# Kernel optimization log

Hardware: AMD Instinct MI355X
Metric: run time of the kernel (lower is better)

The kernel has to match this reference:

```python
import jax, jax.numpy as jnp
import numpy as np

LN_EPS = 1e-12


def setup_inputs() -> dict:
    key = jax.random.key(0)
    ks = jax.random.split(key, 10)
    B, S, W, D, H = 16, 512, 5, 200, 768
    std = 0.02
    return {
        "layer_output": jax.random.normal(ks[0], (B, S, H), dtype=jnp.float32),
        "word_embeddings": jax.random.normal(ks[1], (B, S, W, D), dtype=jnp.float32),
        "word_mask": jax.random.randint(ks[2], (B, S, W), 0, 2, dtype=jnp.int64),
        "W1": jax.random.normal(ks[3], (D, H), dtype=jnp.float32) * std,
        "b1": jnp.zeros((H,), dtype=jnp.float32),
        "W2": jax.random.normal(ks[4], (H, H), dtype=jnp.float32) * std,
        "b2": jnp.zeros((H,), dtype=jnp.float32),
        "attn_W": jax.random.normal(ks[5], (H, H), dtype=jnp.float32) * std,
        "ln_gamma": jnp.ones((H,), dtype=jnp.float32),
        "ln_beta": jnp.zeros((H,), dtype=jnp.float32),
    }


def reference(layer_output, word_embeddings, word_mask, W1, b1, W2, b2, attn_W, ln_gamma, ln_beta):
    # word_transform: Linear -> Tanh -> Linear (dropout = identity in eval)
    we = jnp.tanh(jnp.einsum("bswd,dh->bswh", word_embeddings, W1) + b1)
    we = jnp.einsum("bswh,hk->bswk", we, W2) + b2  # [B,S,W,H]

    # bilinear word attention: (x @ attn_W) . word_outputs -> score over W
    q = jnp.einsum("bsh,hk->bsk", layer_output, attn_W)  # [B,S,H]
    alpha = jnp.einsum("bsk,bswk->bsw", q, we)            # [B,S,W]
    alpha = alpha + (1.0 - word_mask.astype(alpha.dtype)) * -10000.0
    alpha = jax.nn.softmax(alpha, axis=-1)

    # weighted sum over words + residual
    agg = jnp.einsum("bsw,bswh->bsh", alpha, we)
    h = layer_output + agg

    # LayerNorm (fuse_layer; dropout = identity in eval)
    mu = jnp.mean(h, axis=-1, keepdims=True)
    var = jnp.mean(jnp.square(h - mu), axis=-1, keepdims=True)
    return (h - mu) * jax.lax.rsqrt(var + LN_EPS) * ln_gamma + ln_beta
```

## Files before the change

### kernel.cpp

```cpp
#include <hip/hip_runtime.h>
#include <hip/hip_bf16.h>
#include <math.h>


typedef __attribute__((ext_vector_type(8))) short bf16x8;
typedef __attribute__((ext_vector_type(4))) float f32x4;

__device__ __forceinline__ unsigned short f2bf_bits(float f) {
    __hip_bfloat16 h = __float2bfloat16(f);
    return *reinterpret_cast<unsigned short*>(&h);
}
__device__ __forceinline__ float bf_bits2f(unsigned short u) {
    union { unsigned int i; float f; } v; v.i = ((unsigned int)u) << 16; return v.f;
}
__device__ __forceinline__ float tanh_fast(float x) {
    float xc = fminf(fmaxf(x, -9.f), 9.f);
    float t  = __expf(2.f * xc);
    return (t - 1.f) * __builtin_amdgcn_rcpf(t + 1.f);
}

__device__ __forceinline__ void async_cp16(const void* g, void* lds) {
#if __has_builtin(__builtin_amdgcn_global_load_lds)
    auto gp = (const __attribute__((address_space(1))) unsigned int*)g;
    auto lp = (__attribute__((address_space(3))) unsigned int*)lds;
    __builtin_amdgcn_global_load_lds(gp, lp, 16, 0, 0);
#else
    *(uint4*)lds = *(const uint4*)g;
#endif
}

template<bool HAS_BIAS, bool TANH_ACT, bool RESID, bool OUT_BF16, int N, int K, int GX>
__global__ __launch_bounds__(256) void mfma_gemm(
    const __hip_bfloat16* __restrict__ A,
    const __hip_bfloat16* __restrict__ Bt,
    const float* __restrict__ bias,
    const float* __restrict__ resid,
    void* __restrict__ outp)
{
    __shared__ __align__(16) unsigned char smem[32768];
    unsigned short* As = (unsigned short*)smem;
    unsigned short* Bs = (unsigned short*)(smem + 8192);

    int bx, by;
    {
        const int total = gridDim.x;
        const int per_xcd = total >> 3;
        if ((total & 7) == 0 && (per_xcd % GX) == 0) {
            int xcd = blockIdx.x & 7, idx = blockIdx.x >> 3;
            int lin = xcd * per_xcd + idx;
            by = lin / GX; bx = lin % GX;
        } else { by = blockIdx.x / GX; bx = blockIdx.x % GX; }
    }
    const int m0 = by * 128;
    const int n0 = bx * 128;

    const int tid  = threadIdx.x;
    const int lane = tid & 63;
    const int wave = tid >> 6;
    const int wm   = wave & 1;
    const int wn   = wave >> 1;

    const int srow  = lane >> 2;
    const int skoff = (lane & 3) * 8;
    const __hip_bfloat16* gA = A  + (size_t)(m0 + wave * 32 + srow) * K + skoff;
    const __hip_bfloat16* gB = Bt + (size_t)(n0 + wave * 32 + srow) * K + skoff;
    unsigned short* lA = As + wave * 1024 + lane * 8;
    unsigned short* lB = Bs + wave * 1024 + lane * 8;

    const int row16 = lane & 15;
    const int kq    = lane >> 4;

    f32x4 acc[4][4];
#pragma unroll
    for (int i = 0; i < 4; i++)
#pragma unroll
        for (int j = 0; j < 4; j++) acc[i][j] = (f32x4){0.f, 0.f, 0.f, 0.f};

    for (int k0 = 0; k0 < K; k0 += 32) {
        async_cp16(gA,          lA);
        async_cp16(gA + 16 * K, lA + 512);
        async_cp16(gB,          lB);
        async_cp16(gB + 16 * K, lB + 512);
        gA += 32; gB += 32;
        __syncthreads();

        bf16x8 af[4], bg[4];
#pragma unroll
        for (int mi = 0; mi < 4; mi++)
            af[mi] = *(const bf16x8*)&As[(wm * 64 + mi * 16 + row16) * 32 + kq * 8];
#pragma unroll
        for (int ni = 0; ni < 4; ni++)
            bg[ni] = *(const bf16x8*)&Bs[(wn * 64 + ni * 16 + row16) * 32 + kq * 8];
#pragma unroll
        for (int mi = 0; mi < 4; mi++)
#pragma unroll
            for (int ni = 0; ni < 4; ni++)
                acc[mi][ni] = __builtin_amdgcn_mfma_f32_16x16x32_bf16(
                    af[mi], bg[ni], acc[mi][ni], 0, 0, 0);
        __syncthreads();
    }

    if (OUT_BF16) {
        unsigned short* rep = (unsigned short*)smem;
#pragma unroll
        for (int ni = 0; ni < 4; ni++) {
            const int c = wn * 64 + ni * 16 + row16;
            float bcol = HAS_BIAS ? bias[n0 + c] : 0.f;
#pragma unroll
            for (int mi = 0; mi < 4; mi++)
#pragma unroll
                for (int r = 0; r < 4; r++) {
                    const int rr = wm * 64 + mi * 16 + kq * 4 + r;
                    float v = acc[mi][ni][r];
                    if (HAS_BIAS) v += bcol;
                    if (TANH_ACT) v = tanh_fast(v);
                    rep[rr * 128 + c] = f2bf_bits(v);
                }
        }
        __syncthreads();
#pragma unroll
        for (int p = 0; p < 8; p++) {
            const int lin = p * 256 + tid;
            const int row = lin >> 4;
            const int c8  = lin & 15;
            uint4 d = *(const uint4*)&rep[row * 128 + c8 * 8];
            *(uint4*)((__hip_bfloat16*)outp + (size_t)(m0 + row) * N + n0 + c8 * 8) = d;
        }
    } else {
        float* rep = (float*)smem;
#pragma unroll
        for (int h = 0; h < 2; h++) {
            if (wm == h) {
#pragma unroll
                for (int ni = 0; ni < 4; ni++) {
                    const int c = wn * 64 + ni * 16 + row16;
                    float bcol = HAS_BIAS ? bias[n0 + c] : 0.f;
#pragma unroll
                    for (int mi = 0; mi < 4; mi++)
#pragma unroll
                        for (int r = 0; r < 4; r++) {
                            const int rr = mi * 16 + kq * 4 + r;
                            float v = acc[mi][ni][r];
                            if (HAS_BIAS) v += bcol;
                            if (TANH_ACT) v = tanh_fast(v);
                            rep[rr * 128 + c] = v;
                        }
                }
            }
            __syncthreads();
#pragma unroll
            for (int p = 0; p < 8; p++) {
                const int lin = p * 256 + tid;
                const int row = lin >> 5;
                const int c4  = lin & 31;
                float4 v = *(const float4*)&rep[row * 128 + c4 * 4];
                const int grow = m0 + h * 64 + row;
                if (RESID) {
                    float4 rv = *(const float4*)&resid[(size_t)grow * N + n0 + c4 * 4];
                    v.x += rv.x; v.y += rv.y; v.z += rv.z; v.w += rv.w;
                }
                *(float4*)((float*)outp + (size_t)grow * N + n0 + c4 * 4) = v;
            }
            __syncthreads();
        }
    }
}

__global__ __launch_bounds__(256) void cvt_all(
    const float* __restrict__ x,  __hip_bfloat16* __restrict__ xb,
    const float* __restrict__ w2, __hip_bfloat16* __restrict__ w2b,
    const float* __restrict__ aw, __hip_bfloat16* __restrict__ awb)
{
    const int NX = 8192 * 768 / 4;
    const int NW = 768 * 768 / 4;
    long long i = (long long)blockIdx.x * 256 + threadIdx.x;
    const float* src; __hip_bfloat16* dst;
    if (i < NX)           { src = x;  dst = xb;  }
    else if (i < NX + NW) { src = w2; dst = w2b; i -= NX; }
    else                  { src = aw; dst = awb; i -= NX + NW; if (i >= NW) return; }
    float4 v = ((const float4*)src)[i];
    ((ushort4*)dst)[i] = make_ushort4(f2bf_bits(v.x), f2bf_bits(v.y), f2bf_bits(v.z), f2bf_bits(v.w));
}

__global__ __launch_bounds__(256) void cvt_padE(const float* __restrict__ E,
                                                __hip_bfloat16* __restrict__ Eb)
{
    const int lane = threadIdx.x & 63;
    const int wave = threadIdx.x >> 6;
    const long long row = (long long)blockIdx.x * 4 + wave;
    const int k = lane * 4;
    if (k < 224) {
        float4 v = make_float4(0.f, 0.f, 0.f, 0.f);
        if (k < 200) v = *(const float4*)&E[row * 200 + k];
        *(ushort4*)&Eb[row * 224 + k] =
            make_ushort4(f2bf_bits(v.x), f2bf_bits(v.y), f2bf_bits(v.z), f2bf_bits(v.w));
    }
}

__global__ __launch_bounds__(256) void transpose_cvt(const float* __restrict__ in,
                                                     __hip_bfloat16* __restrict__ out,
                                                     int R, int C, int Rpad)
{
    __shared__ float tile[32][33];
    const int c0 = blockIdx.x * 32, r0 = blockIdx.y * 32;
    const int x = threadIdx.x, y = threadIdx.y;
#pragma unroll
    for (int i = 0; i < 32; i += 8) {
        int r = r0 + y + i;
        tile[y + i][x] = (r < R) ? in[(size_t)r * C + c0 + x] : 0.f;
    }
    __syncthreads();
#pragma unroll
    for (int i = 0; i < 32; i += 8)
        out[(size_t)(c0 + y + i) * Rpad + r0 + x] = __float2bfloat16(tile[x][y + i]);
}

__global__ __launch_bounds__(256) void attn_kernel(
    const __hip_bfloat16* __restrict__ T,
    const __hip_bfloat16* P,
    const int* __restrict__ mask,
    __hip_bfloat16* S)
{
    const int lane = threadIdx.x & 63;
    const int wave = threadIdx.x >> 6;
    const int r    = blockIdx.x * 4 + wave;
    const int base = lane * 12;

    float pv[12];
    {
        const ushort4* pp = (const ushort4*)((const unsigned short*)P + (size_t)r * 768 + base);
        ushort4 u0 = pp[0], u1 = pp[1], u2 = pp[2];
        unsigned short us[12] = {u0.x,u0.y,u0.z,u0.w, u1.x,u1.y,u1.z,u1.w, u2.x,u2.y,u2.z,u2.w};
#pragma unroll
        for (int j = 0; j < 12; j++) pv[j] = bf_bits2f(us[j]);
    }
    float tv[5][12], part[5];
#pragma unroll
    for (int w = 0; w < 5; w++) {
        const ushort4* tp = (const ushort4*)((const unsigned short*)T + ((size_t)r * 5 + w) * 768 + base);
        ushort4 u0 = tp[0], u1 = tp[1], u2 = tp[2];
        unsigned short us[12] = {u0.x,u0.y,u0.z,u0.w, u1.x,u1.y,u1.z,u1.w, u2.x,u2.y,u2.z,u2.w};
        float s = 0.f;
#pragma unroll
        for (int j = 0; j < 12; j++) { tv[w][j] = bf_bits2f(us[j]); s += tv[w][j] * pv[j]; }
        part[w] = s;
    }
#pragma unroll
    for (int off = 32; off > 0; off >>= 1)
#pragma unroll
        for (int w = 0; w < 5; w++)
            part[w] += __shfl_xor(part[w], off, 64);

    float logit[5], mx = -1e30f;
#pragma unroll
    for (int w = 0; w < 5; w++) {
        float m = (float)mask[(size_t)r * 5 + w];
        logit[w] = part[w] - 10000.0f * (1.0f - m);
        mx = fmaxf(mx, logit[w]);
    }
    float se = 0.f;
#pragma unroll
    for (int w = 0; w < 5; w++) { logit[w] = expf(logit[w] - mx); se += logit[w]; }
    const float inv = 1.0f / se;

    unsigned short os[12];
#pragma unroll
    for (int j = 0; j < 12; j++) {
        float s = 0.f;
#pragma unroll
        for (int w = 0; w < 5; w++) s += logit[w] * tv[w][j];
        os[j] = f2bf_bits(s * inv);
    }
    ushort4* sp = (ushort4*)((unsigned short*)S + (size_t)r * 768 + base);
    sp[0] = make_ushort4(os[0], os[1], os[2],  os[3]);
    sp[1] = make_ushort4(os[4], os[5], os[6],  os[7]);
    sp[2] = make_ushort4(os[8], os[9], os[10], os[11]);
}

__global__ __launch_bounds__(256) void ln_kernel(
    const float* __restrict__ Hbuf, const float* __restrict__ gamma,
    const float* __restrict__ beta, float* __restrict__ out)
{
    const int lane = threadIdx.x & 63;
    const int wave = threadIdx.x >> 6;
    const int r    = blockIdx.x * 4 + wave;
    const float* hr = Hbuf + (size_t)r * 768 + lane * 12;

    float v[12];
    {
        float4 a = *(const float4*)(hr);
        float4 b = *(const float4*)(hr + 4);
        float4 c = *(const float4*)(hr + 8);
        v[0]=a.x; v[1]=a.y; v[2]=a.z; v[3]=a.w;
        v[4]=b.x; v[5]=b.y; v[6]=b.z; v[7]=b.w;
        v[8]=c.x; v[9]=c.y; v[10]=c.z; v[11]=c.w;
    }
    float s = 0.f;
#pragma unroll
    for (int j = 0; j < 12; j++) s += v[j];
#pragma unroll
    for (int off = 32; off > 0; off >>= 1) s += __shfl_xor(s, off, 64);
    const float mu = s * (1.f / 768.f);
    float vs = 0.f;
#pragma unroll
    for (int j = 0; j < 12; j++) { float d = v[j] - mu; vs += d * d; }
#pragma unroll
    for (int off = 32; off > 0; off >>= 1) vs += __shfl_xor(vs, off, 64);
    const float rs = rsqrtf(vs * (1.f / 768.f) + 1e-12f);

    float o[12];
#pragma unroll
    for (int j = 0; j < 12; j++) {
        int h = lane * 12 + j;
        o[j] = (v[j] - mu) * rs * gamma[h] + beta[h];
    }
    float* orow = out + (size_t)r * 768 + lane * 12;
    *(float4*)(orow)     = make_float4(o[0], o[1], o[2],  o[3]);
    *(float4*)(orow + 4) = make_float4(o[4], o[5], o[6],  o[7]);
    *(float4*)(orow + 8) = make_float4(o[8], o[9], o[10], o[11]);
}

extern "C" void kernel_launch(void* const* d_in, const int* in_sizes, int n_in,
                              void* d_out, int out_size, void* d_ws, size_t ws_size,
                              hipStream_t stream)
{
    const float* x      = (const float*)d_in[0];
    const float* E      = (const float*)d_in[1];
    const int*   mask   = (const int*)d_in[2];
    const float* W1     = (const float*)d_in[3];
    const float* b1     = (const float*)d_in[4];
    const float* W2     = (const float*)d_in[5];
    const float* b2     = (const float*)d_in[6];
    const float* attn_W = (const float*)d_in[7];
    const float* gamma  = (const float*)d_in[8];
    const float* beta   = (const float*)d_in[9];
    float* out = (float*)d_out;

    const int BS = 8192, H = 768, M1 = 40960, KP = 224;

    char* p = (char*)d_ws;
    auto alloc = [&](size_t bytes) { char* q = p; p += (bytes + 255) & ~(size_t)255; return q; };
    __hip_bfloat16* xb    = (__hip_bfloat16*)alloc((size_t)BS * H * 2);
    __hip_bfloat16* W2b   = (__hip_bfloat16*)alloc((size_t)H * H * 2);
    __hip_bfloat16* W2Tb  = (__hip_bfloat16*)alloc((size_t)H * H * 2);
    __hip_bfloat16* attnb = (__hip_bfloat16*)alloc((size_t)H * H * 2);
    __hip_bfloat16* Ctb   = (__hip_bfloat16*)alloc((size_t)H * H * 2);
    __hip_bfloat16* W1Tb  = (__hip_bfloat16*)alloc((size_t)H * KP * 2);
    __hip_bfloat16* Tb    = (__hip_bfloat16*)alloc((size_t)M1 * H * 2);
    __hip_bfloat16* Eb    = (__hip_bfloat16*)alloc((size_t)M1 * KP * 2);
    float* Hb = (float*)Tb;
    __hip_bfloat16* Pb = Eb;
    __hip_bfloat16* Sb = Pb;

    cvt_all<<<6144 + 576 + 576, 256, 0, stream>>>(x, xb, W2, W2b, attn_W, attnb);
    cvt_padE<<<M1 / 4, 256, 0, stream>>>(E, Eb);
    transpose_cvt<<<dim3(24, 7),  dim3(32, 8), 0, stream>>>(W1, W1Tb, 200, H, KP);
    transpose_cvt<<<dim3(24, 24), dim3(32, 8), 0, stream>>>(W2, W2Tb, H, H, H);

    mfma_gemm<false, false, false, true, 768, 768, 6><<<36, 256, 0, stream>>>(
        W2b, attnb, nullptr, nullptr, Ctb);
    mfma_gemm<true, true, false, true, 768, 224, 6><<<1920, 256, 0, stream>>>(
        Eb, W1Tb, b1, nullptr, Tb);
    mfma_gemm<false, false, false, true, 768, 768, 6><<<384, 256, 0, stream>>>(
        xb, Ctb, nullptr, nullptr, Pb);
    attn_kernel<<<BS / 4, 256, 0, stream>>>(Tb, Pb, mask, Sb);
    mfma_gemm<true, false, true, false, 768, 768, 6><<<384, 256, 0, stream>>>(
        Sb, W2Tb, b2, x, Hb);
    ln_kernel<<<BS / 4, 256, 0, stream>>>(Hb, gamma, beta, out);
}
```

Measured before the change: 242.1 us.

## Deepen GEMM K-tile to 64 with XOR-swizzled LDS and fuse prep kernels

```diff
diff --git a/kernel.cpp b/kernel.cpp
--- a/kernel.cpp
+++ b/kernel.cpp
@@ -39,7 +39,7 @@
 {
     __shared__ __align__(16) unsigned char smem[32768];
     unsigned short* As = (unsigned short*)smem;
-    unsigned short* Bs = (unsigned short*)(smem + 8192);
+    unsigned short* Bs = (unsigned short*)(smem + 16384);
 
     int bx, by;
     {
@@ -60,12 +60,13 @@
     const int wm   = wave & 1;
     const int wn   = wave >> 1;
 
-    const int srow  = lane >> 2;
-    const int skoff = (lane & 3) * 8;
-    const __hip_bfloat16* gA = A  + (size_t)(m0 + wave * 32 + srow) * K + skoff;
-    const __hip_bfloat16* gB = Bt + (size_t)(n0 + wave * 32 + srow) * K + skoff;
-    unsigned short* lA = As + wave * 1024 + lane * 8;
-    unsigned short* lB = Bs + wave * 1024 + lane * 8;
+    const int rsub = lane >> 3;
+    const int slot = lane & 7;
+    const int kc   = slot ^ rsub;
+    const __hip_bfloat16* gA = A  + (size_t)(m0 + wave * 32 + rsub) * K + kc * 8;
+    const __hip_bfloat16* gB = Bt + (size_t)(n0 + wave * 32 + rsub) * K + kc * 8;
+    unsigned short* lA = As + wave * 2048 + lane * 8;
+    unsigned short* lB = Bs + wave * 2048 + lane * 8;
 
     const int row16 = lane & 15;
     const int kq    = lane >> 4;
@@ -76,27 +77,39 @@
 #pragma unroll
         for (int j = 0; j < 4; j++) acc[i][j] = (f32x4){0.f, 0.f, 0.f, 0.f};
 
-    for (int k0 = 0; k0 < K; k0 += 32) {
-        async_cp16(gA,          lA);
-        async_cp16(gA + 16 * K, lA + 512);
-        async_cp16(gB,          lB);
-        async_cp16(gB + 16 * K, lB + 512);
-        gA += 32; gB += 32;
+    for (int k0 = 0; k0 < K; k0 += 64) {
+#pragma unroll
+        for (int i = 0; i < 4; i++) {
+            async_cp16(gA + i * 8 * K, lA + i * 512);
+            async_cp16(gB + i * 8 * K, lB + i * 512);
+        }
+        gA += 64; gB += 64;
         __syncthreads();
 
-        bf16x8 af[4], bg[4];
-#pragma unroll
-        for (int mi = 0; mi < 4; mi++)
-            af[mi] = *(const bf16x8*)&As[(wm * 64 + mi * 16 + row16) * 32 + kq * 8];
-#pragma unroll
-        for (int ni = 0; ni < 4; ni++)
-            bg[ni] = *(const bf16x8*)&Bs[(wn * 64 + ni * 16 + row16) * 32 + kq * 8];
-#pragma unroll
-        for (int mi = 0; mi < 4; mi++)
-#pragma unroll
-            for (int ni = 0; ni < 4; ni++)
-                acc[mi][ni] = __builtin_amdgcn_mfma_f32_16x16x32_bf16(
-                    af[mi], bg[ni], acc[mi][ni], 0, 0, 0);
+        bf16x8 af[2][4], bg[2][4];
+#pragma unroll
+        for (int kh = 0; kh < 2; kh++) {
+#pragma unroll
+            for (int mi = 0; mi < 4; mi++) {
+                const int r = wm * 64 + mi * 16 + row16;
+                const int s = (kh * 4 + kq) ^ (r & 7);
+                af[kh][mi] = *(const bf16x8*)&As[r * 64 + s * 8];
+            }
+#pragma unroll
+            for (int ni = 0; ni < 4; ni++) {
+                const int r = wn * 64 + ni * 16 + row16;
+                const int s = (kh * 4 + kq) ^ (r & 7);
+                bg[kh][ni] = *(const bf16x8*)&Bs[r * 64 + s * 8];
+            }
+        }
+#pragma unroll
+        for (int kh = 0; kh < 2; kh++)
+#pragma unroll
+            for (int mi = 0; mi < 4; mi++)
+#pragma unroll
+                for (int ni = 0; ni < 4; ni++)
+                    acc[mi][ni] = __builtin_amdgcn_mfma_f32_16x16x32_bf16(
+                        af[kh][mi], bg[kh][ni], acc[mi][ni], 0, 0, 0);
         __syncthreads();
     }
 
@@ -166,53 +179,47 @@
     }
 }
 
-__global__ __launch_bounds__(256) void cvt_all(
+__global__ __launch_bounds__(256) void prep_kernel(
     const float* __restrict__ x,  __hip_bfloat16* __restrict__ xb,
     const float* __restrict__ w2, __hip_bfloat16* __restrict__ w2b,
-    const float* __restrict__ aw, __hip_bfloat16* __restrict__ awb)
-{
-    const int NX = 8192 * 768 / 4;
-    const int NW = 768 * 768 / 4;
-    long long i = (long long)blockIdx.x * 256 + threadIdx.x;
-    const float* src; __hip_bfloat16* dst;
-    if (i < NX)           { src = x;  dst = xb;  }
-    else if (i < NX + NW) { src = w2; dst = w2b; i -= NX; }
-    else                  { src = aw; dst = awb; i -= NX + NW; if (i >= NW) return; }
-    float4 v = ((const float4*)src)[i];
-    ((ushort4*)dst)[i] = make_ushort4(f2bf_bits(v.x), f2bf_bits(v.y), f2bf_bits(v.z), f2bf_bits(v.w));
-}
-
-__global__ __launch_bounds__(256) void cvt_padE(const float* __restrict__ E,
-                                                __hip_bfloat16* __restrict__ Eb)
-{
-    const int lane = threadIdx.x & 63;
-    const int wave = threadIdx.x >> 6;
-    const long long row = (long long)blockIdx.x * 4 + wave;
-    const int k = lane * 4;
-    if (k < 224) {
+    const float* __restrict__ aw, __hip_bfloat16* __restrict__ awb,
+    const float* __restrict__ E,  __hip_bfloat16* __restrict__ Eb,
+    const float* __restrict__ W1, __hip_bfloat16* __restrict__ W1Tb,
+    __hip_bfloat16* __restrict__ W2Tb)
+{
+    __shared__ float tile[32][33];
+    const int b = blockIdx.x, tid = threadIdx.x;
+    if (b < 6144 + 576 + 576) {
+        const float* src; __hip_bfloat16* dst; long long i;
+        if (b < 6144)      { src = x;  dst = xb;  i = (long long)b * 256 + tid; }
+        else if (b < 6720) { src = w2; dst = w2b; i = (long long)(b - 6144) * 256 + tid; }
+        else               { src = aw; dst = awb; i = (long long)(b - 6720) * 256 + tid; }
+        float4 v = ((const float4*)src)[i];
+        ((ushort4*)dst)[i] = make_ushort4(f2bf_bits(v.x), f2bf_bits(v.y), f2bf_bits(v.z), f2bf_bits(v.w));
+    } else if (b < 7296 + 10240) {
+        const int lane = tid & 63, wave = tid >> 6;
+        const long long row = (long long)(b - 7296) * 4 + wave;
+        const int k = lane * 4;
         float4 v = make_float4(0.f, 0.f, 0.f, 0.f);
         if (k < 200) v = *(const float4*)&E[row * 200 + k];
-        *(ushort4*)&Eb[row * 224 + k] =
+        *(ushort4*)&Eb[row * 256 + k] =
             make_ushort4(f2bf_bits(v.x), f2bf_bits(v.y), f2bf_bits(v.z), f2bf_bits(v.w));
-    }
-}
-
-__global__ __launch_bounds__(256) void transpose_cvt(const float* __restrict__ in,
-                                                     __hip_bfloat16* __restrict__ out,
-                                                     int R, int C, int Rpad)
-{
-    __shared__ float tile[32][33];
-    const int c0 = blockIdx.x * 32, r0 = blockIdx.y * 32;
-    const int x = threadIdx.x, y = threadIdx.y;
-#pragma unroll
-    for (int i = 0; i < 32; i += 8) {
-        int r = r0 + y + i;
-        tile[y + i][x] = (r < R) ? in[(size_t)r * C + c0 + x] : 0.f;
-    }
-    __syncthreads();
-#pragma unroll
-    for (int i = 0; i < 32; i += 8)
-        out[(size_t)(c0 + y + i) * Rpad + r0 + x] = __float2bfloat16(tile[x][y + i]);
+    } else {
+        const float* in; __hip_bfloat16* outb; int R, C, Rpad, t;
+        if (b < 17536 + 192) { t = b - 17536; in = W1; outb = W1Tb; R = 200; C = 768; Rpad = 256; }
+        else                 { t = b - 17728; in = w2; outb = W2Tb; R = 768; C = 768; Rpad = 768; }
+        const int c0 = (t % 24) * 32, r0 = (t / 24) * 32;
+        const int xx = tid & 31, yy = tid >> 5;
+#pragma unroll
+        for (int i = 0; i < 32; i += 8) {
+            int r = r0 + yy + i;
+            tile[yy + i][xx] = (r < R) ? in[(size_t)r * C + c0 + xx] : 0.f;
+        }
+        __syncthreads();
+#pragma unroll
+        for (int i = 0; i < 32; i += 8)
+            outb[(size_t)(c0 + yy + i) * Rpad + r0 + xx] = __float2bfloat16(tile[xx][yy + i]);
+    }
 }
 
 __global__ __launch_bounds__(256) void attn_kernel(
@@ -336,7 +343,7 @@
     const float* beta   = (const float*)d_in[9];
     float* out = (float*)d_out;
 
-    const int BS = 8192, H = 768, M1 = 40960, KP = 224;
+    const int BS = 8192, H = 768, M1 = 40960, KP = 256;
 
     char* p = (char*)d_ws;
     auto alloc = [&](size_t bytes) { char* q = p; p += (bytes + 255) & ~(size_t)255; return q; };
@@ -352,14 +359,12 @@
     __hip_bfloat16* Pb = Eb;
     __hip_bfloat16* Sb = Pb;
 
-    cvt_all<<<6144 + 576 + 576, 256, 0, stream>>>(x, xb, W2, W2b, attn_W, attnb);
-    cvt_padE<<<M1 / 4, 256, 0, stream>>>(E, Eb);
-    transpose_cvt<<<dim3(24, 7),  dim3(32, 8), 0, stream>>>(W1, W1Tb, 200, H, KP);
-    transpose_cvt<<<dim3(24, 24), dim3(32, 8), 0, stream>>>(W2, W2Tb, H, H, H);
+    prep_kernel<<<18304, 256, 0, stream>>>(x, xb, W2, W2b, attn_W, attnb,
+                                           E, Eb, W1, W1Tb, W2Tb);
 
     mfma_gemm<false, false, false, true, 768, 768, 6><<<36, 256, 0, stream>>>(
         W2b, attnb, nullptr, nullptr, Ctb);
-    mfma_gemm<true, true, false, true, 768, 224, 6><<<1920, 256, 0, stream>>>(
+    mfma_gemm<true, true, false, true, 768, 256, 6><<<1920, 256, 0, stream>>>(
         Eb, W1Tb, b1, nullptr, Tb);
     mfma_gemm<false, false, false, true, 768, 768, 6><<<384, 256, 0, stream>>>(
         xb, Ctb, nullptr, nullptr, Pb);
```

After: 234.0 us. 1.03x faster.
